# Optimization experiments

Measured on AMD Instinct MI355X. Metric: run time of the kernel, lower is better.

Reference implementation:

```python
import jax, jax.numpy as jnp
import numpy as np

HEADS = 16
D_MODEL = 1024
D_HEAD = D_MODEL // HEADS


def setup_inputs() -> dict:
    key = jax.random.key(0)
    ks = jax.random.split(key, 9)
    s_h = 1.0 / np.sqrt(D_HEAD)
    s_m = 1.0 / np.sqrt(D_MODEL)
    return {
        "x": jax.random.normal(ks[0], (4, 2048, D_MODEL), dtype=jnp.float32),
        "Wq": jax.random.uniform(ks[1], (D_HEAD, D_HEAD), jnp.float32, -s_h, s_h),
        "bq": jax.random.uniform(ks[2], (D_HEAD,), jnp.float32, -s_h, s_h),
        "Wk": jax.random.uniform(ks[3], (D_HEAD, D_HEAD), jnp.float32, -s_h, s_h),
        "bk": jax.random.uniform(ks[4], (D_HEAD,), jnp.float32, -s_h, s_h),
        "Wv": jax.random.uniform(ks[5], (D_HEAD, D_HEAD), jnp.float32, -s_h, s_h),
        "bv": jax.random.uniform(ks[6], (D_HEAD,), jnp.float32, -s_h, s_h),
        "Wp": jax.random.uniform(ks[7], (D_MODEL, D_MODEL), jnp.float32, -s_m, s_m),
        "bp": jax.random.uniform(ks[8], (D_MODEL,), jnp.float32, -s_m, s_m),
    }


def reference(x, Wq, bq, Wk, bk, Wv, bv, Wp, bp):
    B, T, C = x.shape
    xh = x.reshape(B, T, HEADS, D_HEAD)  # [B,T,H,Dh]
    # per-head linear projections (torch Linear: x @ W.T + b)
    q = jnp.einsum('bthd,ed->bhte', xh, Wq) + bq  # [B,H,T,Dh]
    k = jnp.einsum('bthd,ed->bhte', xh, Wk) + bk
    v = jnp.einsum('bthd,ed->bhte', xh, Wv) + bv
    # NOTE: original scales by sqrt(C) = sqrt(d_model), not sqrt(d_head)
    att = jnp.einsum('bhqd,bhkd->bhqk', q, k) / jnp.sqrt(jnp.float32(C))
    att = jax.nn.softmax(att, axis=-1)
    out = jnp.einsum('bhqk,bhkd->bhqd', att, v)  # [B,H,T,Dh]
    out = out.transpose(0, 2, 1, 3).reshape(B, T, C)
    return out @ Wp.T + bp
```

## Files before the change

kernel.cpp:

```cpp
#include <hip/hip_runtime.h>
#include <hip/hip_bf16.h>
#include <cstddef>

#define B_  4
#define T_  2048
#define H_  16
#define DH  64
#define C_  1024
#define BH  64

typedef float  f32x16 __attribute__((ext_vector_type(16)));
typedef __bf16 bf16x8 __attribute__((ext_vector_type(8)));
typedef __bf16 bf16x4 __attribute__((ext_vector_type(4)));

#define MFMA32(a, b, c) __builtin_amdgcn_mfma_f32_32x32x16_bf16(a, b, c, 0, 0, 0)


__device__ __forceinline__ unsigned cvt_pk_bf16(float lo, float hi) {
    unsigned r;
    asm("v_cvt_pk_bf16_f32 %0, %1, %2" : "=v"(r) : "v"(lo), "v"(hi));
    return r;
}

__global__ __launch_bounds__(256) void wconv_kernel(
    const float* __restrict__ Wq, const float* __restrict__ Wk,
    const float* __restrict__ Wv, __bf16* __restrict__ wqkv)
{
    const int tid = blockIdx.x * 256 + threadIdx.x;
    const float* srcs[3] = {Wq, Wk, Wv};
    const int mat = tid >> 10;
    const int off = (tid & 1023) * 4;
    const float4 w4 = *(const float4*)(srcs[mat] + off);
    const unsigned lo = ((unsigned)__builtin_bit_cast(unsigned short, (__bf16)w4.y) << 16)
                      | (unsigned)__builtin_bit_cast(unsigned short, (__bf16)w4.x);
    const unsigned hi = ((unsigned)__builtin_bit_cast(unsigned short, (__bf16)w4.w) << 16)
                      | (unsigned)__builtin_bit_cast(unsigned short, (__bf16)w4.z);
    uint2 p; p.x = lo; p.y = hi;
    *(uint2*)(wqkv + mat * 4096 + off) = p;
}

__global__ __launch_bounds__(256) void qkv_kernel(
    const float* __restrict__ x,
    const __bf16* __restrict__ wqkv,
    const float* __restrict__ bq, const float* __restrict__ bk,
    const float* __restrict__ bv,
    __bf16* __restrict__ q, __bf16* __restrict__ kf, __bf16* __restrict__ vf)
{
    __shared__ __bf16 Xs[128 * 72];
    __shared__ __bf16 Ws[3][64 * 72];
    __bf16* Vtl = Xs;
    __bf16* Kst = &Ws[0][0];

    const int tt  = blockIdx.x;
    const int bh  = blockIdx.y;
    const int b   = bh >> 4, h = bh & 15;
    const int t0  = tt * 128;
    const int tid = threadIdx.x;
    const int wave = tid >> 6, lane = tid & 63;
    const int m = lane & 31, hh = lane >> 5;

    #pragma unroll
    for (int i = 0; i < 8; ++i) {
        const int idx = i * 256 + tid;
        const int r = idx >> 4, c = (idx & 15) * 4;
        const float4 x4 = *(const float4*)(x + ((size_t)(b * T_ + t0 + r)) * C_ + h * DH + c);
        const unsigned lo = ((unsigned)__builtin_bit_cast(unsigned short, (__bf16)x4.y) << 16)
                          | (unsigned)__builtin_bit_cast(unsigned short, (__bf16)x4.x);
        const unsigned hi = ((unsigned)__builtin_bit_cast(unsigned short, (__bf16)x4.w) << 16)
                          | (unsigned)__builtin_bit_cast(unsigned short, (__bf16)x4.z);
        *(unsigned*)&Xs[r * 72 + c]     = lo;
        *(unsigned*)&Xs[r * 72 + c + 2] = hi;
    }
    #pragma unroll
    for (int i = 0; i < 6; ++i) {
        const int idx = i * 256 + tid;
        const int mat_ = idx >> 9;
        const int r = (idx >> 3) & 63, c = (idx & 7) * 8;
        *(uint4*)&Ws[mat_][r * 72 + c] = *(const uint4*)(wqkv + mat_ * 4096 + r * 64 + c);
    }
    __syncthreads();

    bf16x8 xf[4];
    #pragma unroll
    for (int ks = 0; ks < 4; ++ks)
        xf[ks] = *(const bf16x8*)&Xs[(wave * 32 + m) * 72 + ks * 16 + hh * 8];
    __syncthreads();

    const float s32 = 0.03125f * 1.4426950408889634f;

    unsigned kpk[16];

    #pragma unroll
    for (int mat = 0; mat < 3; ++mat) {
        f32x16 acc0 = {}, acc1 = {};
        #pragma unroll
        for (int ks = 0; ks < 4; ++ks) {
            const bf16x8 w0 = *(const bf16x8*)&Ws[mat][(m) * 72 + ks * 16 + hh * 8];
            const bf16x8 w1 = *(const bf16x8*)&Ws[mat][(32 + m) * 72 + ks * 16 + hh * 8];
            acc0 = MFMA32(xf[ks], w0, acc0);
            acc1 = MFMA32(xf[ks], w1, acc1);
        }
        const float* bias = (mat == 0) ? bq : (mat == 1) ? bk : bv;
        const float b0 = bias[m], b1 = bias[32 + m];
        #pragma unroll
        for (int r = 0; r < 16; ++r) {
            const int R = (r & 3) + 8 * (r >> 2) + 4 * hh;
            const int tloc = wave * 32 + R;
            const float v0 = acc0[r] + b0, v1 = acc1[r] + b1;
            if (mat == 0) {
                const size_t base = ((size_t)bh * T_ + t0 + tloc) * DH;
                q[base + m]      = (__bf16)(v0 * s32);
                q[base + 32 + m] = (__bf16)(v1 * s32);
            } else if (mat == 1) {
                kpk[r] = ((unsigned)__builtin_bit_cast(unsigned short, (__bf16)v1) << 16)
                       |  (unsigned)__builtin_bit_cast(unsigned short, (__bf16)v0);
            } else {
                Vtl[(m) * 136 + tloc]      = (__bf16)v0;
                Vtl[(32 + m) * 136 + tloc] = (__bf16)v1;
            }
        }
    }
    __syncthreads();

    #pragma unroll
    for (int r = 0; r < 16; ++r) {
        const int R = (r & 3) + 8 * (r >> 2) + 4 * hh;
        const int tloc = wave * 32 + R;
        Kst[tloc * 72 + m]      = __builtin_bit_cast(__bf16, (unsigned short)(kpk[r] & 0xffff));
        Kst[tloc * 72 + 32 + m] = __builtin_bit_cast(__bf16, (unsigned short)(kpk[r] >> 16));
    }

    #pragma unroll
    for (int i = 0; i < 4; ++i) {
        const int idx = i * 256 + tid;
        const int ln = idx & 63, c_ = idx >> 6;
        const int kt64l = c_ >> 3, dh = (c_ >> 2) & 1, cN = c_ & 3;
        const __bf16* src = &Vtl[(dh * 32 + (ln & 31)) * 136 + kt64l * 64 + cN * 16 + (ln >> 5) * 8];
        __bf16* dst = vf + ((((size_t)(bh * 32 + tt * 2 + kt64l) * 2 + dh) * 4 + cN) * 64 + ln) * 8;
        *(uint4*)dst = *(const uint4*)src;
    }
    __syncthreads();

    #pragma unroll
    for (int i = 0; i < 4; ++i) {
        const int idx = i * 256 + tid;
        const int ln = idx & 63, c_ = idx >> 6;
        const int kt64l = c_ >> 3, rh = (c_ >> 2) & 1, ks = c_ & 3;
        const __bf16* src = &Kst[(kt64l * 64 + rh * 32 + (ln & 31)) * 72 + ks * 16 + (ln >> 5) * 8];
        __bf16* dst = kf + ((((size_t)(bh * 32 + tt * 2 + kt64l) * 2 + rh) * 4 + ks) * 64 + ln) * 8;
        *(uint4*)dst = *(const uint4*)src;
    }
}

__global__ __launch_bounds__(256, 4) void attn_kernel(
    const __bf16* __restrict__ q, const __bf16* __restrict__ kf,
    const __bf16* __restrict__ vf, __bf16* __restrict__ af)
{
    __shared__ __bf16 Os[128 * 72];

    const int bh  = blockIdx.x;
    const int q0  = blockIdx.y * 128;
    const int tid = threadIdx.x;
    const int wave = tid >> 6, lane = tid & 63;
    const int m = lane & 31, h = lane >> 5;

    const __bf16* qb  = q  + (size_t)bh * T_ * DH;
    const __bf16* kfb = kf + (size_t)bh * (T_ * DH);
    const __bf16* vfb = vf + (size_t)bh * (T_ * DH);

    bf16x8 qf[4];
    #pragma unroll
    for (int ks = 0; ks < 4; ++ks)
        qf[ks] = *(const bf16x8*)(qb + (size_t)(q0 + wave * 32 + m) * DH + ks * 16 + h * 8);

    f32x16 O0 = {}, O1 = {};
    float lsum = 0.f;

    for (int kt = 0; kt < 32; ++kt) {
        const __bf16* kt_k = kfb + kt * 4096;
        const __bf16* kt_v = vfb + kt * 4096;
        #pragma unroll
        for (int rh = 0; rh < 2; ++rh) {
            bf16x8 kfr[4];
            #pragma unroll
            for (int ks = 0; ks < 4; ++ks)
                kfr[ks] = *(const bf16x8*)(kt_k + rh * 2048 + ks * 512 + lane * 8);
            f32x16 S = {};
            #pragma unroll
            for (int ks = 0; ks < 4; ++ks)
                S = MFMA32(kfr[ks], qf[ks], S);

            #pragma unroll
            for (int cc = 0; cc < 2; ++cc) {
                const int rb = cc * 8;
                float e0 = __builtin_amdgcn_exp2f(S[rb + 0]);
                float e1 = __builtin_amdgcn_exp2f(S[rb + 1]);
                float e2 = __builtin_amdgcn_exp2f(S[rb + 2]);
                float e3 = __builtin_amdgcn_exp2f(S[rb + 3]);
                float e4 = __builtin_amdgcn_exp2f(S[rb + 4]);
                float e5 = __builtin_amdgcn_exp2f(S[rb + 5]);
                float e6 = __builtin_amdgcn_exp2f(S[rb + 6]);
                float e7 = __builtin_amdgcn_exp2f(S[rb + 7]);
                lsum += ((e0 + e1) + (e2 + e3)) + ((e4 + e5) + (e6 + e7));
                unsigned a0 = cvt_pk_bf16(e0, e1);
                unsigned a1 = cvt_pk_bf16(e2, e3);
                unsigned b0 = cvt_pk_bf16(e4, e5);
                unsigned b1 = cvt_pk_bf16(e6, e7);
                asm("v_permlane32_swap_b32 %0, %1" : "+v"(a0), "+v"(b0));
                asm("v_permlane32_swap_b32 %0, %1" : "+v"(a1), "+v"(b1));
                const uint4 pw = {a0, a1, b0, b1};
                const bf16x8 pb = __builtin_bit_cast(bf16x8, pw);
                const int c = rh * 2 + cc;
                const bf16x8 v0 = *(const bf16x8*)(kt_v + c * 512 + lane * 8);
                const bf16x8 v1 = *(const bf16x8*)(kt_v + 2048 + c * 512 + lane * 8);
                O0 = MFMA32(v0, pb, O0);
                O1 = MFMA32(v1, pb, O1);
            }
        }
    }

    lsum += __shfl_xor(lsum, 32);
    const float linv = 1.0f / lsum;

    #pragma unroll
    for (int g = 0; g < 4; ++g) {
        bf16x4 w0, w1;
        #pragma unroll
        for (int j = 0; j < 4; ++j) {
            w0[j] = (__bf16)(O0[4 * g + j] * linv);
            w1[j] = (__bf16)(O1[4 * g + j] * linv);
        }
        const int row = (wave * 32 + m) * 72;
        *(bf16x4*)&Os[row + 8 * g + 4 * h]      = w0;
        *(bf16x4*)&Os[row + 32 + 8 * g + 4 * h] = w1;
    }
    __syncthreads();

    __bf16* ab = af + ((size_t)(bh * 16 + (q0 >> 7))) * 8192;
    #pragma unroll
    for (int i = 0; i < 4; ++i) {
        const int idx = i * 256 + tid;
        const int ln = idx & 63, c_ = idx >> 6;
        const int wv = c_ >> 2, ks = c_ & 3;
        const __bf16* src = &Os[(wv * 32 + (ln & 31)) * 72 + ks * 16 + (ln >> 5) * 8];
        *(uint4*)(ab + c_ * 512 + ln * 8) = *(const uint4*)src;
    }
}

__global__ __launch_bounds__(256) void wpconv_kernel(
    const float* __restrict__ Wp, __bf16* __restrict__ wpf)
{
    const int gtid = blockIdx.x * 256 + threadIdx.x;
    #pragma unroll
    for (int i = 0; i < 4; ++i) {
        const int ci = gtid + i * 32768;
        const int ln = ci & 63;
        const int ks = (ci >> 6) & 3;
        const int n  = (ci >> 8) & 3;
        const int cb = (ci >> 10) & 15;
        const int eb = ci >> 14;
        const int row = eb * 128 + n * 32 + (ln & 31);
        const int col = cb * 64 + ks * 16 + (ln >> 5) * 8;
        const float4 w0 = *(const float4*)(Wp + (size_t)row * C_ + col);
        const float4 w1 = *(const float4*)(Wp + (size_t)row * C_ + col + 4);
        uint4 p;
        p.x = ((unsigned)__builtin_bit_cast(unsigned short, (__bf16)w0.y) << 16)
            |  (unsigned)__builtin_bit_cast(unsigned short, (__bf16)w0.x);
        p.y = ((unsigned)__builtin_bit_cast(unsigned short, (__bf16)w0.w) << 16)
            |  (unsigned)__builtin_bit_cast(unsigned short, (__bf16)w0.z);
        p.z = ((unsigned)__builtin_bit_cast(unsigned short, (__bf16)w1.y) << 16)
            |  (unsigned)__builtin_bit_cast(unsigned short, (__bf16)w1.x);
        p.w = ((unsigned)__builtin_bit_cast(unsigned short, (__bf16)w1.w) << 16)
            |  (unsigned)__builtin_bit_cast(unsigned short, (__bf16)w1.z);
        *(uint4*)(wpf + (size_t)ci * 8) = p;
    }
}

__global__ __launch_bounds__(256) void proj_kernel(
    const __bf16* __restrict__ af,
    const __bf16* __restrict__ wpf,
    const float* __restrict__ bp,
    float* __restrict__ out)
{
    const int tb = blockIdx.x, eb = blockIdx.y;
    const int tid = threadIdx.x;
    const int wave = tid >> 6, lane = tid & 63;
    const int m = lane & 31, h = lane >> 5;
    const int tok0 = tb * 128;
    const int b = tb >> 4, qtile = tb & 15;
    const int e0 = eb * 128;

    const __bf16* abase = af + ((size_t)(b * 256 + qtile)) * 8192
                             + (wave * 4) * 512 + lane * 8;
    const __bf16* wbase = wpf + (size_t)eb * 131072 + lane * 8;

    f32x16 acc[4] = {f32x16{}, f32x16{}, f32x16{}, f32x16{}};

    for (int cb = 0; cb < 16; ++cb) {
        const __bf16* ap = abase + (size_t)cb * 131072;
        const __bf16* wp = wbase + (size_t)cb * 8192;
        bf16x8 afr[4];
        #pragma unroll
        for (int ks = 0; ks < 4; ++ks)
            afr[ks] = *(const bf16x8*)(ap + ks * 512);
        #pragma unroll
        for (int n = 0; n < 4; ++n) {
            #pragma unroll
            for (int ks = 0; ks < 4; ++ks) {
                const bf16x8 bf = *(const bf16x8*)(wp + (n * 4 + ks) * 512);
                acc[n] = MFMA32(afr[ks], bf, acc[n]);
            }
        }
    }

    #pragma unroll
    for (int n = 0; n < 4; ++n) {
        const int e = e0 + n * 32 + m;
        const float bias = bp[e];
        #pragma unroll
        for (int r = 0; r < 16; ++r) {
            const int R = (r & 3) + 8 * (r >> 2) + 4 * h;
            out[(size_t)(tok0 + wave * 32 + R) * C_ + e] = acc[n][r] + bias;
        }
    }
}

extern "C" void kernel_launch(void* const* d_in, const int* in_sizes, int n_in,
                              void* d_out, int out_size, void* d_ws, size_t ws_size,
                              hipStream_t stream)
{
    const float* x  = (const float*)d_in[0];
    const float* Wq = (const float*)d_in[1];
    const float* bq = (const float*)d_in[2];
    const float* Wk = (const float*)d_in[3];
    const float* bk = (const float*)d_in[4];
    const float* Wv = (const float*)d_in[5];
    const float* bv = (const float*)d_in[6];
    const float* Wp = (const float*)d_in[7];
    const float* bp = (const float*)d_in[8];

    const size_t N = (size_t)BH * T_ * DH;
    __bf16* qws  = (__bf16*)d_ws;
    __bf16* kws  = qws + N;
    __bf16* vtws = kws + N;
    __bf16* aws  = vtws + N;
    __bf16* wqkv = aws;
    __bf16* wpf  = qws;

    wconv_kernel<<<dim3(12), 256, 0, stream>>>(Wq, Wk, Wv, wqkv);
    qkv_kernel<<<dim3(16, 64), 256, 0, stream>>>(
        x, wqkv, bq, bk, bv, qws, kws, vtws);
    attn_kernel<<<dim3(64, 16), 256, 0, stream>>>(qws, kws, vtws, aws);
    wpconv_kernel<<<dim3(128), 256, 0, stream>>>(Wp, wpf);
    proj_kernel<<<dim3(64, 8), 256, 0, stream>>>(aws, wpf, bp, (float*)d_out);
}
```

Baseline: 248.7 us.

## Split attention KV range across waves and double grid sizes for attn/proj

Attention blocks now cover 64 queries, and the two wave pairs each process half of the key range (split-K). Their partial O and row sums are combined through shared memory, and the output is written directly from registers with permlane swaps. The projection kernel is split so each block handles half the tokens and each wave pair half the output columns, doubling the grid. Weight conversion uses one element per thread with a larger grid. The aim is more blocks to fill the CUs, at the cost of extra reduction work and more redundant K/V and weight loads.

```diff
diff --git a/kernel.cpp b/kernel.cpp
--- a/kernel.cpp
+++ b/kernel.cpp
@@ -156,13 +156,16 @@
     const __bf16* __restrict__ q, const __bf16* __restrict__ kf,
     const __bf16* __restrict__ vf, __bf16* __restrict__ af)
 {
-    __shared__ __bf16 Os[128 * 72];
+    __shared__ float OL[2][64 * 36];
+    __shared__ float LL[2][64];
 
     const int bh  = blockIdx.x;
-    const int q0  = blockIdx.y * 128;
+    const int q0  = blockIdx.y * 64;
     const int tid = threadIdx.x;
     const int wave = tid >> 6, lane = tid & 63;
     const int m = lane & 31, h = lane >> 5;
+    const int qs  = wave & 1;
+    const int kvh = wave >> 1;
 
     const __bf16* qb  = q  + (size_t)bh * T_ * DH;
     const __bf16* kfb = kf + (size_t)bh * (T_ * DH);
@@ -171,12 +174,13 @@
     bf16x8 qf[4];
     #pragma unroll
     for (int ks = 0; ks < 4; ++ks)
-        qf[ks] = *(const bf16x8*)(qb + (size_t)(q0 + wave * 32 + m) * DH + ks * 16 + h * 8);
+        qf[ks] = *(const bf16x8*)(qb + (size_t)(q0 + qs * 32 + m) * DH + ks * 16 + h * 8);
 
     f32x16 O0 = {}, O1 = {};
     float lsum = 0.f;
 
-    for (int kt = 0; kt < 32; ++kt) {
+    const int ktEnd = kvh * 16 + 16;
+    for (int kt = kvh * 16; kt < ktEnd; ++kt) {
         const __bf16* kt_k = kfb + kt * 4096;
         const __bf16* kt_v = vfb + kt * 4096;
         #pragma unroll
@@ -219,61 +223,75 @@
         }
     }
 
-    lsum += __shfl_xor(lsum, 32);
-    const float linv = 1.0f / lsum;
-
-    #pragma unroll
-    for (int g = 0; g < 4; ++g) {
-        bf16x4 w0, w1;
-        #pragma unroll
-        for (int j = 0; j < 4; ++j) {
-            w0[j] = (__bf16)(O0[4 * g + j] * linv);
-            w1[j] = (__bf16)(O1[4 * g + j] * linv);
-        }
-        const int row = (wave * 32 + m) * 72;
-        *(bf16x4*)&Os[row + 8 * g + 4 * h]      = w0;
-        *(bf16x4*)&Os[row + 32 + 8 * g + 4 * h] = w1;
-    }
-    __syncthreads();
-
-    __bf16* ab = af + ((size_t)(bh * 16 + (q0 >> 7))) * 8192;
-    #pragma unroll
-    for (int i = 0; i < 4; ++i) {
-        const int idx = i * 256 + tid;
-        const int ln = idx & 63, c_ = idx >> 6;
-        const int wv = c_ >> 2, ks = c_ & 3;
-        const __bf16* src = &Os[(wv * 32 + (ln & 31)) * 72 + ks * 16 + (ln >> 5) * 8];
-        *(uint4*)(ab + c_ * 512 + ln * 8) = *(const uint4*)src;
+    if (kvh == 1) {
+        #pragma unroll
+        for (int g = 0; g < 4; ++g) {
+            float4 p0, p1;
+            p0.x = O0[4 * g];     p0.y = O0[4 * g + 1];
+            p0.z = O0[4 * g + 2]; p0.w = O0[4 * g + 3];
+            p1.x = O1[4 * g];     p1.y = O1[4 * g + 1];
+            p1.z = O1[4 * g + 2]; p1.w = O1[4 * g + 3];
+            *(float4*)&OL[qs][lane * 36 + 4 * g]      = p0;
+            *(float4*)&OL[qs][lane * 36 + 16 + 4 * g] = p1;
+        }
+        LL[qs][lane] = lsum;
+    }
+    __syncthreads();
+    if (kvh == 0) {
+        #pragma unroll
+        for (int g = 0; g < 4; ++g) {
+            const float4 p0 = *(const float4*)&OL[qs][lane * 36 + 4 * g];
+            const float4 p1 = *(const float4*)&OL[qs][lane * 36 + 16 + 4 * g];
+            O0[4 * g]     += p0.x; O0[4 * g + 1] += p0.y;
+            O0[4 * g + 2] += p0.z; O0[4 * g + 3] += p0.w;
+            O1[4 * g]     += p1.x; O1[4 * g + 1] += p1.y;
+            O1[4 * g + 2] += p1.z; O1[4 * g + 3] += p1.w;
+        }
+        lsum += LL[qs][lane];
+        lsum += __shfl_xor(lsum, 32);
+        const float linv = 1.0f / lsum;
+
+        __bf16* ab = af + ((size_t)(bh * 16 + (q0 >> 7))) * 8192
+                        + (((q0 >> 6) & 1) * 2 + qs) * 2048 + lane * 8;
+        #pragma unroll
+        for (int ks = 0; ks < 4; ++ks) {
+            const f32x16& Og = (ks < 2) ? O0 : O1;
+            const int rb = (ks & 1) * 8;
+            unsigned a0 = cvt_pk_bf16(Og[rb + 0] * linv, Og[rb + 1] * linv);
+            unsigned a1 = cvt_pk_bf16(Og[rb + 2] * linv, Og[rb + 3] * linv);
+            unsigned b0 = cvt_pk_bf16(Og[rb + 4] * linv, Og[rb + 5] * linv);
+            unsigned b1 = cvt_pk_bf16(Og[rb + 6] * linv, Og[rb + 7] * linv);
+            asm("v_permlane32_swap_b32 %0, %1" : "+v"(a0), "+v"(b0));
+            asm("v_permlane32_swap_b32 %0, %1" : "+v"(a1), "+v"(b1));
+            const uint4 pw = {a0, a1, b0, b1};
+            *(uint4*)(ab + ks * 512) = pw;
+        }
     }
 }
 
 __global__ __launch_bounds__(256) void wpconv_kernel(
     const float* __restrict__ Wp, __bf16* __restrict__ wpf)
 {
-    const int gtid = blockIdx.x * 256 + threadIdx.x;
-    #pragma unroll
-    for (int i = 0; i < 4; ++i) {
-        const int ci = gtid + i * 32768;
-        const int ln = ci & 63;
-        const int ks = (ci >> 6) & 3;
-        const int n  = (ci >> 8) & 3;
-        const int cb = (ci >> 10) & 15;
-        const int eb = ci >> 14;
-        const int row = eb * 128 + n * 32 + (ln & 31);
-        const int col = cb * 64 + ks * 16 + (ln >> 5) * 8;
-        const float4 w0 = *(const float4*)(Wp + (size_t)row * C_ + col);
-        const float4 w1 = *(const float4*)(Wp + (size_t)row * C_ + col + 4);
-        uint4 p;
-        p.x = ((unsigned)__builtin_bit_cast(unsigned short, (__bf16)w0.y) << 16)
-            |  (unsigned)__builtin_bit_cast(unsigned short, (__bf16)w0.x);
-        p.y = ((unsigned)__builtin_bit_cast(unsigned short, (__bf16)w0.w) << 16)
-            |  (unsigned)__builtin_bit_cast(unsigned short, (__bf16)w0.z);
-        p.z = ((unsigned)__builtin_bit_cast(unsigned short, (__bf16)w1.y) << 16)
-            |  (unsigned)__builtin_bit_cast(unsigned short, (__bf16)w1.x);
-        p.w = ((unsigned)__builtin_bit_cast(unsigned short, (__bf16)w1.w) << 16)
-            |  (unsigned)__builtin_bit_cast(unsigned short, (__bf16)w1.z);
-        *(uint4*)(wpf + (size_t)ci * 8) = p;
-    }
+    const int ci = blockIdx.x * 256 + threadIdx.x;
+    const int ln = ci & 63;
+    const int ks = (ci >> 6) & 3;
+    const int n  = (ci >> 8) & 3;
+    const int cb = (ci >> 10) & 15;
+    const int eb = ci >> 14;
+    const int row = eb * 128 + n * 32 + (ln & 31);
+    const int col = cb * 64 + ks * 16 + (ln >> 5) * 8;
+    const float4 w0 = *(const float4*)(Wp + (size_t)row * C_ + col);
+    const float4 w1 = *(const float4*)(Wp + (size_t)row * C_ + col + 4);
+    uint4 p;
+    p.x = ((unsigned)__builtin_bit_cast(unsigned short, (__bf16)w0.y) << 16)
+        |  (unsigned)__builtin_bit_cast(unsigned short, (__bf16)w0.x);
+    p.y = ((unsigned)__builtin_bit_cast(unsigned short, (__bf16)w0.w) << 16)
+        |  (unsigned)__builtin_bit_cast(unsigned short, (__bf16)w0.z);
+    p.z = ((unsigned)__builtin_bit_cast(unsigned short, (__bf16)w1.y) << 16)
+        |  (unsigned)__builtin_bit_cast(unsigned short, (__bf16)w1.x);
+    p.w = ((unsigned)__builtin_bit_cast(unsigned short, (__bf16)w1.w) << 16)
+        |  (unsigned)__builtin_bit_cast(unsigned short, (__bf16)w1.z);
+    *(uint4*)(wpf + (size_t)ci * 8) = p;
 }
 
 __global__ __launch_bounds__(256) void proj_kernel(
@@ -282,19 +300,21 @@
     const float* __restrict__ bp,
     float* __restrict__ out)
 {
-    const int tb = blockIdx.x, eb = blockIdx.y;
+    const int tb2 = blockIdx.x, eb = blockIdx.y;
     const int tid = threadIdx.x;
     const int wave = tid >> 6, lane = tid & 63;
     const int m = lane & 31, h = lane >> 5;
-    const int tok0 = tb * 128;
-    const int b = tb >> 4, qtile = tb & 15;
+    const int b = tb2 >> 5, rem = tb2 & 31;
+    const int qtile = rem >> 1, half = rem & 1;
+    const int wv = half * 2 + (wave & 1);
+    const int eh = wave >> 1;
     const int e0 = eb * 128;
 
     const __bf16* abase = af + ((size_t)(b * 256 + qtile)) * 8192
-                             + (wave * 4) * 512 + lane * 8;
-    const __bf16* wbase = wpf + (size_t)eb * 131072 + lane * 8;
-
-    f32x16 acc[4] = {f32x16{}, f32x16{}, f32x16{}, f32x16{}};
+                             + wv * 2048 + lane * 8;
+    const __bf16* wbase = wpf + (size_t)eb * 131072 + eh * 4096 + lane * 8;
+
+    f32x16 acc[2] = {f32x16{}, f32x16{}};
 
     for (int cb = 0; cb < 16; ++cb) {
         const __bf16* ap = abase + (size_t)cb * 131072;
@@ -304,7 +324,7 @@
         for (int ks = 0; ks < 4; ++ks)
             afr[ks] = *(const bf16x8*)(ap + ks * 512);
         #pragma unroll
-        for (int n = 0; n < 4; ++n) {
+        for (int n = 0; n < 2; ++n) {
             #pragma unroll
             for (int ks = 0; ks < 4; ++ks) {
                 const bf16x8 bf = *(const bf16x8*)(wp + (n * 4 + ks) * 512);
@@ -313,14 +333,15 @@
         }
     }
 
-    #pragma unroll
-    for (int n = 0; n < 4; ++n) {
-        const int e = e0 + n * 32 + m;
+    const int tokbase = b * T_ + qtile * 128 + wv * 32;
+    #pragma unroll
+    for (int n = 0; n < 2; ++n) {
+        const int e = e0 + (eh * 2 + n) * 32 + m;
         const float bias = bp[e];
         #pragma unroll
         for (int r = 0; r < 16; ++r) {
             const int R = (r & 3) + 8 * (r >> 2) + 4 * h;
-            out[(size_t)(tok0 + wave * 32 + R) * C_ + e] = acc[n][r] + bias;
+            out[(size_t)(tokbase + R) * C_ + e] = acc[n][r] + bias;
         }
     }
 }
@@ -350,7 +371,7 @@
     wconv_kernel<<<dim3(12), 256, 0, stream>>>(Wq, Wk, Wv, wqkv);
     qkv_kernel<<<dim3(16, 64), 256, 0, stream>>>(
         x, wqkv, bq, bk, bv, qws, kws, vtws);
-    attn_kernel<<<dim3(64, 16), 256, 0, stream>>>(qws, kws, vtws, aws);
-    wpconv_kernel<<<dim3(128), 256, 0, stream>>>(Wp, wpf);
-    proj_kernel<<<dim3(64, 8), 256, 0, stream>>>(aws, wpf, bp, (float*)d_out);
-}
+    attn_kernel<<<dim3(64, 32), 256, 0, stream>>>(qws, kws, vtws, aws);
+    wpconv_kernel<<<dim3(512), 256, 0, stream>>>(Wp, wpf);
+    proj_kernel<<<dim3(128, 8), 256, 0, stream>>>(aws, wpf, bp, (float*)d_out);
+}
```

New measurement: 230.1 us. 7.5% less time.
